# Performance work log

Measured on AMD Instinct MI355X. Metric: run time of the kernel, lower is better.

Reference implementation:

```python
import jax, jax.numpy as jnp
import numpy as np

DN = ('NCHW', 'OIHW', 'NCHW')

def conv3x3(x, w):
    # stride-1, SAME padding, no bias (matches build_conv_layer(..., 3, stride=1, padding='same', bias=False))
    return jax.lax.conv_general_dilated(x, w, window_strides=(1, 1), padding='SAME', dimension_numbers=DN)

def setup_inputs() -> dict:
    key = jax.random.key(0)
    k1, k2, k3, k4 = jax.random.split(key, 4)
    B, C, H, W = 4, 256, 64, 64
    inputs = jax.random.normal(k1, (B, C, H, W), dtype=jnp.float32)
    ref = jax.random.normal(k2, (B, C, H, W), dtype=jnp.float32)
    # xavier-uniform-ish conv weights, [O, I, kH, kW]
    fan = C * 9
    lim = np.sqrt(6.0 / (fan + fan)).astype(np.float32)
    w1 = jax.random.uniform(k3, (C, C, 3, 3), dtype=jnp.float32, minval=-lim, maxval=lim)
    w2 = jax.random.uniform(k4, (C, C, 3, 3), dtype=jnp.float32, minval=-lim, maxval=lim)
    gamma = jnp.float32(0.5)
    return {'inputs': inputs, 'ref': ref, 'w1': w1, 'w2': w2, 'gamma': gamma}

def reference(inputs, ref, w1, w2, gamma):
    # Faithful to source: x0 = relu(conv1(inputs)) is computed then immediately
    # overwritten by a view of x1 (a bug in the original), so inputs only
    # contributes its shape. We execute the dead conv for FLOP parity.
    _dead = jax.nn.relu(conv3x3(inputs, w1))
    x1 = jax.nn.relu(conv3x3(ref, w1))            # [B, C, H, W]
    B, C, H, W = x1.shape
    q = x1.transpose(0, 2, 3, 1).reshape(B, H * W, C)   # [B, HW, C]
    k = x1.reshape(B, C, H * W)                          # [B, C, HW]
    scores = jnp.einsum('bnc,bcm->bnm', q, k)            # [B, HW, HW]
    corr = jax.nn.softmax(scores, axis=1)                # softmax over dim=1 (atypical axis)
    v = jax.nn.relu(conv3x3(ref, w2)).reshape(B, C, H * W)  # [B, C, HW]
    A = jnp.einsum('bcn,bnm->bcm', v, corr).reshape(inputs.shape)
    return A * gamma + ref
```

## Files before the change

kernel.cpp:

```cpp
#include <hip/hip_runtime.h>
#include <math.h>

#define CDIM 256
#define NSEQ 4096
#define HWDIM 64
#define PPIX 4356

typedef unsigned short u16;
typedef __attribute__((ext_vector_type(8))) short bf16x8;
typedef __attribute__((ext_vector_type(4))) float f32x4;
typedef __attribute__((ext_vector_type(16))) float f32x16;

__device__ __forceinline__ u16 f2bf(float f) {
    unsigned u = __float_as_uint(f);
    unsigned r = (u + 0x7FFFu + ((u >> 16) & 1u)) >> 16;
    return (u16)r;
}

__device__ __forceinline__ void gload_lds16(const u16* g, u16* l) {
    __builtin_amdgcn_global_load_lds(
        (const __attribute__((address_space(1))) unsigned int*)g,
        (__attribute__((address_space(3))) unsigned int*)l, 16, 0, 0);
}

__global__ __launch_bounds__(256)
void pad_transpose_kernel(const float* __restrict__ x, u16* __restrict__ padded)
{
    __shared__ float lds[64 * 65];
    const int tid = threadIdx.x;
    const int y = blockIdx.x, c0 = blockIdx.y << 6, b = blockIdx.z;
    #pragma unroll
    for (int i = 0; i < 16; ++i) {
        int f = tid + (i << 8);
        int c = f >> 6, xx = f & 63;
        lds[c * 65 + xx] = x[(((size_t)(b * CDIM + c0 + c)) * HWDIM + y) * HWDIM + xx];
    }
    __syncthreads();
    #pragma unroll
    for (int i = 0; i < 2; ++i) {
        int f = tid + (i << 8);
        int xx = f >> 3, c8 = f & 7;
        union { u16 h[8]; float4 v; } pk;
        #pragma unroll
        for (int j = 0; j < 8; ++j) pk.h[j] = f2bf(lds[(c8 * 8 + j) * 65 + xx]);
        *(float4*)&padded[((size_t)b * PPIX + (y + 1) * 66 + (xx + 1)) * CDIM + c0 + (c8 << 3)] = pk.v;
    }
}

__global__ __launch_bounds__(256)
void w_prepack_kernel(const float* __restrict__ w, u16* __restrict__ wk)
{
    int t = (blockIdx.x << 8) + threadIdx.x;
    const float* wp = w + (size_t)t * 9;
    #pragma unroll
    for (int j = 0; j < 9; ++j) wk[j * 65536 + t] = f2bf(wp[j]);
}

template <bool OA>
__global__ __launch_bounds__(256)
void conv_mfma_kernel(const u16* __restrict__ padded, const u16* __restrict__ wk,
                      u16* __restrict__ out)
{
    __shared__ alignas(16) u16 Xs[64 * 64];
    __shared__ alignas(16) u16 Ws[128 * 64];

    const int tid = threadIdx.x;
    const int lane = tid & 63, wv = tid >> 6;
    const int lr = lane & 15, lg = lane >> 4;
    const int cb = blockIdx.x << 7;
    const int y0 = blockIdx.y;
    const int b = blockIdx.z;

    constexpr int MF = OA ? 4 : 2;
    constexpr int NF = OA ? 2 : 4;
    f32x4 acc[MF][NF] = {};

    for (int t = 0; t < 36; ++t) {
        const int kyx = t >> 2, cib = (t & 3) << 6;
        const int ky = kyx / 3, kx = kyx - ky * 3;
        __syncthreads();
        #pragma unroll
        for (int i = 0; i < 2; ++i) {
            int f = tid + (i << 8);
            int r = f >> 3, c8 = f & 7;
            int pp = (y0 + ky) * 66 + r + kx;
            float4 v = *(const float4*)&padded[((size_t)b * PPIX + pp) * CDIM + cib + (c8 << 3)];
            *(float4*)&Xs[(r << 6) + ((c8 << 3) ^ ((r & 7) << 3))] = v;
        }
        #pragma unroll
        for (int i = 0; i < 4; ++i) {
            int f = tid + (i << 8);
            int r = f >> 3, c8 = f & 7;
            float4 v = *(const float4*)&wk[((size_t)kyx << 16) + (size_t)(cb + r) * 256 + cib + (c8 << 3)];
            *(float4*)&Ws[(r << 6) + ((c8 << 3) ^ ((r & 7) << 3))] = v;
        }
        __syncthreads();
        #pragma unroll
        for (int kk = 0; kk < 2; ++kk) {
            const int ca = ((kk << 5) + (lg << 3)) ^ ((lr & 7) << 3);
            if constexpr (OA) {
                bf16x8 a[4], bb[2];
                #pragma unroll
                for (int mf = 0; mf < 4; ++mf)
                    a[mf] = *(const bf16x8*)&Xs[((mf * 16 + lr) << 6) + ca];
                #pragma unroll
                for (int nf = 0; nf < 2; ++nf)
                    bb[nf] = *(const bf16x8*)&Ws[((wv * 32 + nf * 16 + lr) << 6) + ca];
                #pragma unroll
                for (int mf = 0; mf < 4; ++mf)
                    #pragma unroll
                    for (int nf = 0; nf < 2; ++nf)
                        acc[mf][nf] = __builtin_amdgcn_mfma_f32_16x16x32_bf16(a[mf], bb[nf], acc[mf][nf], 0, 0, 0);
            } else {
                bf16x8 a[2], bb[4];
                #pragma unroll
                for (int mf = 0; mf < 2; ++mf)
                    a[mf] = *(const bf16x8*)&Ws[((wv * 32 + mf * 16 + lr) << 6) + ca];
                #pragma unroll
                for (int nf = 0; nf < 4; ++nf)
                    bb[nf] = *(const bf16x8*)&Xs[((nf * 16 + lr) << 6) + ca];
                #pragma unroll
                for (int mf = 0; mf < 2; ++mf)
                    #pragma unroll
                    for (int nf = 0; nf < 4; ++nf)
                        acc[mf][nf] = __builtin_amdgcn_mfma_f32_16x16x32_bf16(a[mf], bb[nf], acc[mf][nf], 0, 0, 0);
            }
        }
    }

    const int m0 = y0 << 6;
    if constexpr (OA) {
        #pragma unroll
        for (int mf = 0; mf < 4; ++mf)
            #pragma unroll
            for (int nf = 0; nf < 2; ++nf) {
                int nb = m0 + mf * 16 + lg * 4;
                int co = cb + wv * 32 + nf * 16 + lr;
                union { u16 h[4]; uint2 v; } pk;
                #pragma unroll
                for (int j = 0; j < 4; ++j) pk.h[j] = f2bf(fmaxf(acc[mf][nf][j], 0.f));
                *(uint2*)&out[((size_t)(b * CDIM + co)) * NSEQ + nb] = pk.v;
            }
    } else {
        #pragma unroll
        for (int mf = 0; mf < 2; ++mf)
            #pragma unroll
            for (int nf = 0; nf < 4; ++nf) {
                int cob = cb + wv * 32 + mf * 16 + lg * 4;
                int n = m0 + nf * 16 + lr;
                union { u16 h[4]; uint2 v; } pk;
                #pragma unroll
                for (int j = 0; j < 4; ++j) pk.h[j] = f2bf(fmaxf(acc[mf][nf][j], 0.f));
                *(uint2*)&out[((size_t)(b * NSEQ + n)) * CDIM + cob] = pk.v;
            }
    }
}

#define M_TILE 128
#define NC 64
#define NCHUNKS 32

#define KS_OFF 0
#define VS_OFF 32768
#define P_OFF  65536
#define SM_OFF 73728

__device__ __forceinline__ void stage_chunk(const u16* __restrict__ XT, const u16* __restrict__ Vn,
                                            u16* Kb, u16* Vb, int b, int n0, int wv, int lane)
{
    #pragma unroll
    for (int i = 0; i < 4; ++i) {
        int f = ((i << 3) + wv) << 6;
        int fl = f + lane;
        int r = fl >> 5;
        int gsw = (fl & 31) ^ (r & 15);
        gload_lds16(&XT[(size_t)(b * NSEQ + n0 + r) * CDIM + (gsw << 3)], Kb + (f << 3));
    }
    #pragma unroll
    for (int i = 0; i < 4; ++i) {
        int f = ((i << 3) + wv) << 6;
        int fl = f + lane;
        int r = fl >> 3;
        int gsw = (fl & 7) ^ (r & 7);
        gload_lds16(&Vn[(size_t)(b * CDIM + r) * NSEQ + n0 + (gsw << 3)], Vb + (f << 3));
    }
}

__global__ __launch_bounds__(512, 2)
void attn_part_kernel(const u16* __restrict__ XT, const u16* __restrict__ Vn,
                      float* __restrict__ o0, u16* __restrict__ o1,
                      float* __restrict__ ml)
{
    __shared__ alignas(16) u16 smem[75008];
    u16* Ps = smem + P_OFF;
    float* cmax_s = (float*)(smem + SM_OFF);
    float* psum_s = cmax_s + 256;
    float* al_s   = psum_s + 256;

    const int tid = threadIdx.x;
    const int lane = tid & 63;
    const int wv = tid >> 6;
    const int l31 = lane & 31;
    const int hi = lane >> 5;
    const int bh = blockIdx.x;
    const int b = bh >> 1, h = bh & 1;
    const int m0 = blockIdx.y * M_TILE;
    const int nbase = h * (NSEQ / 2);

    const int qt = wv & 3;
    const int kh = wv >> 2;
    const int qa = qt * 32 + l31;
    const int qsel = wv & 1;
    const int csel = wv >> 1;

    bf16x8 qreg[16];
    {
        const u16* qrow = &XT[(size_t)(b * NSEQ + m0 + qa) * CDIM + (hi << 3)];
        #pragma unroll
        for (int ks = 0; ks < 16; ++ks)
            qreg[ks] = *(const bf16x8*)(qrow + (ks << 4));
    }

    f32x16 o[2][2] = {};
    float mrun = -INFINITY, lrun = 0.f;

    stage_chunk(XT, Vn, smem + KS_OFF, smem + VS_OFF, b, nbase, wv, lane);
    __syncthreads();

    int cur = 0;
    for (int ci = 0; ci < NCHUNKS; ++ci) {
        if (ci + 1 < NCHUNKS)
            stage_chunk(XT, Vn, smem + KS_OFF + (cur ^ 1) * 16384,
                        smem + VS_OFF + (cur ^ 1) * 16384,
                        b, nbase + (ci + 1) * NC, wv, lane);

        const u16* Kc = smem + KS_OFF + cur * 16384;
        const u16* Vc = smem + VS_OFF + cur * 16384;

        f32x16 s = {};
        {
            const int krow = kh * 32 + l31;
            const u16* kbase = &Kc[krow << 8];
            const int ksw = krow & 15;
            #pragma unroll
            for (int ks = 0; ks < 16; ++ks) {
                bf16x8 ka = *(const bf16x8*)&kbase[(((ks << 1) + hi) ^ ksw) << 3];
                s = __builtin_amdgcn_mfma_f32_32x32x16_bf16(ka, qreg[ks], s, 0, 0, 0);
            }
        }

        float cm = s[0];
        #pragma unroll
        for (int r = 1; r < 16; ++r) cm = fmaxf(cm, s[r]);
        cm = fmaxf(cm, __shfl_xor(cm, 32));
        if (lane < 32) cmax_s[((qt << 1) + kh) * 32 + l31] = cm;
        __syncthreads();

        float cmo = cmax_s[((qt << 1) + (kh ^ 1)) * 32 + l31];
        float mnew = fmaxf(mrun, fmaxf(cm, cmo));
        float al = __expf(mrun - mnew);
        float p[16];
        float ps = 0.f;
        #pragma unroll
        for (int r = 0; r < 16; ++r) { p[r] = __expf(s[r] - mnew); ps += p[r]; }
        ps += __shfl_xor(ps, 32);
        if (lane < 32) {
            psum_s[((qt << 1) + kh) * 32 + l31] = ps;
            if (kh == 0) al_s[qa] = al;
        }
        {
            const int swz = qa & 7;
            #pragma unroll
            for (int r4 = 0; r4 < 4; ++r4) {
                union { u16 h4[4]; uint2 v; } pk;
                pk.h4[0] = f2bf(p[r4 * 4 + 0]); pk.h4[1] = f2bf(p[r4 * 4 + 1]);
                pk.h4[2] = f2bf(p[r4 * 4 + 2]); pk.h4[3] = f2bf(p[r4 * 4 + 3]);
                int g = (kh << 2) + r4;
                *(uint2*)&Ps[(qa << 6) + (((g ^ swz) << 3) | (hi << 2))] = pk.v;
            }
        }
        __syncthreads();
        lrun = lrun * al + ps + psum_s[((qt << 1) + (kh ^ 1)) * 32 + l31];
        mrun = mnew;

        {
            float alv0 = al_s[((qsel << 1) + 0) * 32 + l31];
            float alv1 = al_s[((qsel << 1) + 1) * 32 + l31];
            o[0][0] *= alv0; o[0][1] *= alv0;
            o[1][0] *= alv1; o[1][1] *= alv1;
            const int q0 = ((qsel << 1) + 0) * 32 + l31;
            const int q1 = ((qsel << 1) + 1) * 32 + l31;
            const int c0 = ((csel << 1) + 0) * 32 + l31;
            const int c1 = ((csel << 1) + 1) * 32 + l31;
            #pragma unroll
            for (int ks = 0; ks < 4; ++ks) {
                const int gp = (ks << 1) + hi;
                bf16x8 pb0 = *(const bf16x8*)&Ps[(q0 << 6) + ((gp ^ (q0 & 7)) << 3)];
                bf16x8 pb1 = *(const bf16x8*)&Ps[(q1 << 6) + ((gp ^ (q1 & 7)) << 3)];
                bf16x8 va0 = *(const bf16x8*)&Vc[(c0 << 6) + ((gp ^ (c0 & 7)) << 3)];
                bf16x8 va1 = *(const bf16x8*)&Vc[(c1 << 6) + ((gp ^ (c1 & 7)) << 3)];
                o[0][0] = __builtin_amdgcn_mfma_f32_32x32x16_bf16(va0, pb0, o[0][0], 0, 0, 0);
                o[0][1] = __builtin_amdgcn_mfma_f32_32x32x16_bf16(va1, pb0, o[0][1], 0, 0, 0);
                o[1][0] = __builtin_amdgcn_mfma_f32_32x32x16_bf16(va0, pb1, o[1][0], 0, 0, 0);
                o[1][1] = __builtin_amdgcn_mfma_f32_32x32x16_bf16(va1, pb1, o[1][1], 0, 0, 0);
            }
        }

        __syncthreads();
        cur ^= 1;
    }

    if (kh == 0 && lane < 32) {
        size_t idx = ((size_t)((h * 4 + b) * NSEQ) + m0 + qa) * 2;
        ml[idx] = mrun;
        ml[idx + 1] = lrun;
    }

    #pragma unroll
    for (int qi = 0; qi < 2; ++qi) {
        const int q = m0 + ((qsel << 1) + qi) * 32 + l31;
        #pragma unroll
        for (int cj = 0; cj < 2; ++cj) {
            #pragma unroll
            for (int reg = 0; reg < 16; ++reg) {
                int c = ((csel << 1) + cj) * 32 + (reg & 3) + ((reg >> 2) << 3) + (hi << 2);
                size_t oi = ((size_t)(b * CDIM + c)) * NSEQ + q;
                if (h == 0) o0[oi] = o[qi][cj][reg];
                else        o1[oi] = f2bf(o[qi][cj][reg]);
            }
        }
    }
}

__global__ __launch_bounds__(256)
void merge_kernel(float* __restrict__ out, const u16* __restrict__ o1,
                  const float* __restrict__ ml, const float* __restrict__ ref,
                  const float* __restrict__ gptr)
{
    const int f = (blockIdx.x << 8) + threadIdx.x;
    const int n4 = f & 1023;
    const int c = (f >> 10) & 255;
    const int b = f >> 18;
    const float g = gptr[0];

    float4 p0 = ((const float4*)out)[f];
    uint2 q1 = *(const uint2*)&o1[((size_t)(b * CDIM + c)) * NSEQ + (n4 << 2)];
    float4 rf = ((const float4*)ref)[f];

    float res[4];
    #pragma unroll
    for (int j = 0; j < 4; ++j) {
        int row = (n4 << 2) + j;
        size_t i0 = ((size_t)(0 + b) * NSEQ + row) * 2;
        size_t i1 = ((size_t)(4 + b) * NSEQ + row) * 2;
        float m0 = ml[i0], l0 = ml[i0 + 1];
        float m1 = ml[i1], l1 = ml[i1 + 1];
        float mm = fmaxf(m0, m1);
        float w0 = __expf(m0 - mm), w1 = __expf(m1 - mm);
        float rl = 1.0f / (l0 * w0 + l1 * w1);
        float v0 = ((const float*)&p0)[j];
        unsigned hu = ((j & 1) ? ((&q1.x)[j >> 1] >> 16) : ((&q1.x)[j >> 1] & 0xFFFFu));
        float v1 = __uint_as_float(hu << 16);
        float a = (v0 * w0 + v1 * w1) * rl;
        res[j] = g * a + ((const float*)&rf)[j];
    }
    ((float4*)out)[f] = *(float4*)res;
}

extern "C" void kernel_launch(void* const* d_in, const int* in_sizes, int n_in,
                              void* d_out, int out_size, void* d_ws, size_t ws_size,
                              hipStream_t stream)
{
    const float* ref = (const float*)d_in[1];
    const float* w1  = (const float*)d_in[2];
    const float* w2  = (const float*)d_in[3];
    const float* gma = (const float*)d_in[4];
    float* out = (float*)d_out;

    u16* XT     = (u16*)d_ws;
    u16* Vn     = XT + (size_t)4 * NSEQ * CDIM;
    u16* padded = Vn + (size_t)4 * NSEQ * CDIM;
    u16* wk1    = padded + (size_t)4 * PPIX * CDIM;
    u16* wk2    = wk1 + (size_t)9 * 65536;
    u16*   o1  = padded;
    float* ml  = (float*)wk1;

    hipMemsetAsync(padded, 0, (size_t)4 * PPIX * CDIM * sizeof(u16), stream);
    pad_transpose_kernel<<<dim3(64, 4, 4), 256, 0, stream>>>(ref, padded);
    w_prepack_kernel<<<dim3(256), 256, 0, stream>>>(w1, wk1);
    w_prepack_kernel<<<dim3(256), 256, 0, stream>>>(w2, wk2);

    dim3 cgrid(2, 64, 4);
    conv_mfma_kernel<false><<<cgrid, 256, 0, stream>>>(padded, wk1, XT);
    conv_mfma_kernel<true ><<<cgrid, 256, 0, stream>>>(padded, wk2, Vn);

    attn_part_kernel<<<dim3(8, NSEQ / M_TILE), 512, 0, stream>>>(XT, Vn, out, o1, ml);
    merge_kernel<<<dim3((4 * CDIM * NSEQ / 4) / 256), 256, 0, stream>>>(out, o1, ml, ref, gma);
}
```

Before: 190.7 us.

## Replace online softmax max with a Cauchy-Schwarz bound from row norms

Adds a small kernel that computes the squared norm of every projected row and, per batch, the maximum squared norm (via atomicMax). The attention kernel then uses the fixed per-query offset |q|·max|k| in place of a running softmax maximum. This removes the per-chunk max reduction, two shared-memory exchanges and barriers, and the rescaling of the output accumulators; the merge kernel becomes a plain sum of partial denominators. The trade-off is numerical: if the bound is far above the true maximum score, exp() can underflow and the denominators can lose precision or reach zero.

```diff
diff --git a/kernel.cpp b/kernel.cpp
--- a/kernel.cpp
+++ b/kernel.cpp
@@ -156,6 +156,30 @@
     }
 }
 
+__global__ __launch_bounds__(256)
+void rownorm_kernel(const u16* __restrict__ XT, float* __restrict__ rn2,
+                    unsigned* __restrict__ maxrn2)
+{
+    const int tid = threadIdx.x;
+    const int lane = tid & 63, wv = tid >> 6;
+    const int row = (blockIdx.x << 2) + wv;
+    const u16* xp = &XT[(size_t)row * CDIM + (lane << 2)];
+    uint2 v = *(const uint2*)xp;
+    float s = 0.f;
+    #pragma unroll
+    for (int j = 0; j < 4; ++j) {
+        unsigned hu = (j & 1) ? ((&v.x)[j >> 1] >> 16) : ((&v.x)[j >> 1] & 0xFFFFu);
+        float x = __uint_as_float(hu << 16);
+        s += x * x;
+    }
+    #pragma unroll
+    for (int off = 1; off < 64; off <<= 1) s += __shfl_xor(s, off);
+    if (lane == 0) {
+        rn2[row] = s;
+        atomicMax(&maxrn2[row >> 12], __float_as_uint(s));
+    }
+}
+
 #define M_TILE 128
 #define NC 64
 #define NCHUNKS 32
@@ -163,7 +187,6 @@
 #define KS_OFF 0
 #define VS_OFF 32768
 #define P_OFF  65536
-#define SM_OFF 73728
 
 __device__ __forceinline__ void stage_chunk(const u16* __restrict__ XT, const u16* __restrict__ Vn,
                                             u16* Kb, u16* Vb, int b, int n0, int wv, int lane)
@@ -188,14 +211,12 @@
 
 __global__ __launch_bounds__(512, 2)
 void attn_part_kernel(const u16* __restrict__ XT, const u16* __restrict__ Vn,
+                      const float* __restrict__ rn2, const unsigned* __restrict__ maxrn2,
                       float* __restrict__ o0, u16* __restrict__ o1,
-                      float* __restrict__ ml)
-{
-    __shared__ alignas(16) u16 smem[75008];
+                      float* __restrict__ lsum)
+{
+    __shared__ alignas(16) u16 smem[73728];
     u16* Ps = smem + P_OFF;
-    float* cmax_s = (float*)(smem + SM_OFF);
-    float* psum_s = cmax_s + 256;
-    float* al_s   = psum_s + 256;
 
     const int tid = threadIdx.x;
     const int lane = tid & 63;
@@ -213,6 +234,9 @@
     const int qsel = wv & 1;
     const int csel = wv >> 1;
 
+    const float mq = sqrtf(rn2[(size_t)b * NSEQ + m0 + qa]) *
+                     sqrtf(__uint_as_float(maxrn2[b]));
+
     bf16x8 qreg[16];
     {
         const u16* qrow = &XT[(size_t)(b * NSEQ + m0 + qa) * CDIM + (hi << 3)];
@@ -222,7 +246,7 @@
     }
 
     f32x16 o[2][2] = {};
-    float mrun = -INFINITY, lrun = 0.f;
+    float lrun = 0.f;
 
     stage_chunk(XT, Vn, smem + KS_OFF, smem + VS_OFF, b, nbase, wv, lane);
     __syncthreads();
@@ -249,25 +273,13 @@
             }
         }
 
-        float cm = s[0];
-        #pragma unroll
-        for (int r = 1; r < 16; ++r) cm = fmaxf(cm, s[r]);
-        cm = fmaxf(cm, __shfl_xor(cm, 32));
-        if (lane < 32) cmax_s[((qt << 1) + kh) * 32 + l31] = cm;
-        __syncthreads();
-
-        float cmo = cmax_s[((qt << 1) + (kh ^ 1)) * 32 + l31];
-        float mnew = fmaxf(mrun, fmaxf(cm, cmo));
-        float al = __expf(mrun - mnew);
         float p[16];
         float ps = 0.f;
         #pragma unroll
-        for (int r = 0; r < 16; ++r) { p[r] = __expf(s[r] - mnew); ps += p[r]; }
+        for (int r = 0; r < 16; ++r) { p[r] = __expf(s[r] - mq); ps += p[r]; }
         ps += __shfl_xor(ps, 32);
-        if (lane < 32) {
-            psum_s[((qt << 1) + kh) * 32 + l31] = ps;
-            if (kh == 0) al_s[qa] = al;
-        }
+        lrun += ps;
+
         {
             const int swz = qa & 7;
             #pragma unroll
@@ -280,14 +292,8 @@
             }
         }
         __syncthreads();
-        lrun = lrun * al + ps + psum_s[((qt << 1) + (kh ^ 1)) * 32 + l31];
-        mrun = mnew;
 
         {
-            float alv0 = al_s[((qsel << 1) + 0) * 32 + l31];
-            float alv1 = al_s[((qsel << 1) + 1) * 32 + l31];
-            o[0][0] *= alv0; o[0][1] *= alv0;
-            o[1][0] *= alv1; o[1][1] *= alv1;
             const int q0 = ((qsel << 1) + 0) * 32 + l31;
             const int q1 = ((qsel << 1) + 1) * 32 + l31;
             const int c0 = ((csel << 1) + 0) * 32 + l31;
@@ -310,11 +316,8 @@
         cur ^= 1;
     }
 
-    if (kh == 0 && lane < 32) {
-        size_t idx = ((size_t)((h * 4 + b) * NSEQ) + m0 + qa) * 2;
-        ml[idx] = mrun;
-        ml[idx + 1] = lrun;
-    }
+    if (lane < 32)
+        lsum[(size_t)(((h * 2 + kh) * 4 + b)) * NSEQ + m0 + qa] = lrun;
 
     #pragma unroll
     for (int qi = 0; qi < 2; ++qi) {
@@ -334,7 +337,7 @@
 
 __global__ __launch_bounds__(256)
 void merge_kernel(float* __restrict__ out, const u16* __restrict__ o1,
-                  const float* __restrict__ ml, const float* __restrict__ ref,
+                  const float* __restrict__ lsum, const float* __restrict__ ref,
                   const float* __restrict__ gptr)
 {
     const int f = (blockIdx.x << 8) + threadIdx.x;
@@ -351,17 +354,15 @@
     #pragma unroll
     for (int j = 0; j < 4; ++j) {
         int row = (n4 << 2) + j;
-        size_t i0 = ((size_t)(0 + b) * NSEQ + row) * 2;
-        size_t i1 = ((size_t)(4 + b) * NSEQ + row) * 2;
-        float m0 = ml[i0], l0 = ml[i0 + 1];
-        float m1 = ml[i1], l1 = ml[i1 + 1];
-        float mm = fmaxf(m0, m1);
-        float w0 = __expf(m0 - mm), w1 = __expf(m1 - mm);
-        float rl = 1.0f / (l0 * w0 + l1 * w1);
+        float l = lsum[(size_t)(0 * 4 + b) * NSEQ + row]
+                + lsum[(size_t)(1 * 4 + b) * NSEQ + row]
+                + lsum[(size_t)(2 * 4 + b) * NSEQ + row]
+                + lsum[(size_t)(3 * 4 + b) * NSEQ + row];
+        float rl = 1.0f / l;
         float v0 = ((const float*)&p0)[j];
         unsigned hu = ((j & 1) ? ((&q1.x)[j >> 1] >> 16) : ((&q1.x)[j >> 1] & 0xFFFFu));
         float v1 = __uint_as_float(hu << 16);
-        float a = (v0 * w0 + v1 * w1) * rl;
+        float a = (v0 + v1) * rl;
         res[j] = g * a + ((const float*)&rf)[j];
     }
     ((float4*)out)[f] = *(float4*)res;
@@ -382,8 +383,10 @@
     u16* padded = Vn + (size_t)4 * NSEQ * CDIM;
     u16* wk1    = padded + (size_t)4 * PPIX * CDIM;
     u16* wk2    = wk1 + (size_t)9 * 65536;
-    u16*   o1  = padded;
-    float* ml  = (float*)wk1;
+    u16*      o1     = padded;
+    float*    lsum   = (float*)wk1;
+    float*    rn2    = (float*)wk2;
+    unsigned* maxrn2 = (unsigned*)(wk2 + 65536);
 
     hipMemsetAsync(padded, 0, (size_t)4 * PPIX * CDIM * sizeof(u16), stream);
     pad_transpose_kernel<<<dim3(64, 4, 4), 256, 0, stream>>>(ref, padded);
@@ -394,6 +397,9 @@
     conv_mfma_kernel<false><<<cgrid, 256, 0, stream>>>(padded, wk1, XT);
     conv_mfma_kernel<true ><<<cgrid, 256, 0, stream>>>(padded, wk2, Vn);
 
-    attn_part_kernel<<<dim3(8, NSEQ / M_TILE), 512, 0, stream>>>(XT, Vn, out, o1, ml);
-    merge_kernel<<<dim3((4 * CDIM * NSEQ / 4) / 256), 256, 0, stream>>>(out, o1, ml, ref, gma);
-}
+    hipMemsetAsync(maxrn2, 0, 4 * sizeof(unsigned), stream);
+    rownorm_kernel<<<dim3(4096), 256, 0, stream>>>(XT, rn2, maxrn2);
+
+    attn_part_kernel<<<dim3(8, NSEQ / M_TILE), 512, 0, stream>>>(XT, Vn, rn2, maxrn2, out, o1, lsum);
+    merge_kernel<<<dim3((4 * CDIM * NSEQ / 4) / 256), 256, 0, stream>>>(out, o1, lsum, ref, gma);
+}
```

Result: slower. 368.2 us (+93.1%).
